# Kernel tuning notes

Measured on AMD Instinct MI355X. Metric: run time of the kernel, lower is better.

The kernel has to match this reference:

```python
import jax, jax.numpy as jnp
import numpy as np

N = 163842        # icosphere level-7 vertex count
IN_FEATS = 64
OUT_FEATS = 64
K = 7             # fixed neighborhood size (self + 6 ring neighbors)


def setup_inputs() -> dict:
    key = jax.random.key(0)
    k1, k2, k3, k4 = jax.random.split(key, 4)
    x = jax.random.normal(k1, (N, IN_FEATS), dtype=jnp.float32)
    neigh_orders = jax.random.randint(k2, (K * N,), 0, N, dtype=jnp.int64)
    # torch nn.Linear(7*in, out): weight [out, 7*in], bias [out]
    W = jax.random.normal(k3, (OUT_FEATS, K * IN_FEATS), dtype=jnp.float32) * 0.05
    b = jax.random.normal(k4, (OUT_FEATS,), dtype=jnp.float32) * 0.05
    return {"x": x, "neigh_orders": neigh_orders, "W": W, "b": b}


def reference(x, neigh_orders, W, b):
    # Gather neighbor features: [7*N, in] -> [N, 7*in]
    mat = x[neigh_orders].reshape(x.shape[0], -1)
    # Linear: mat @ W.T + b -> [N, out]
    return jnp.einsum("nk,ok->no", mat, W) + b
```

## Files before the change

kernel.cpp:

```cpp
#include <hip/hip_runtime.h>
#include <hip/hip_bf16.h>

#define NV     163842
#define KTOT   448
#define KQ     56
#define XUNITS (NV * 64 / 8)
#define WQUADS (64 * KTOT / 4)
#define XB_BYTES ((size_t)NV * 64 * 2)
#define WB_BYTES (KQ * 64 * 16)

typedef __attribute__((ext_vector_type(8))) short bf16x8;
typedef __attribute__((ext_vector_type(4))) float f32x4;

__device__ __forceinline__ unsigned f2bf(float f) {
    unsigned u = __builtin_bit_cast(unsigned, f);
    return (u + 0x7FFFu + ((u >> 16) & 1u)) >> 16;
}
__device__ __forceinline__ unsigned pack2(float a, float b) {
    return f2bf(a) | (f2bf(b) << 16);
}

__global__ __launch_bounds__(256) void prep_kernel(
    const float* __restrict__ x, const float* __restrict__ W,
    unsigned char* __restrict__ ws)
{
    const int g = blockIdx.x * 256 + threadIdx.x;
    if (g < XUNITS) {
        const float4 lo = *reinterpret_cast<const float4*>(x + (size_t)g * 8);
        const float4 hi = *reinterpret_cast<const float4*>(x + (size_t)g * 8 + 4);
        uint4 u;
        u.x = pack2(lo.x, lo.y); u.y = pack2(lo.z, lo.w);
        u.z = pack2(hi.x, hi.y); u.w = pack2(hi.z, hi.w);
        *reinterpret_cast<uint4*>(ws + (size_t)g * 16) = u;
    } else if (g < XUNITS + WQUADS) {
        const int q = g - XUNITS;
        const int i = q << 2;
        const int o = i / KTOT;
        const int k = i - o * KTOT;
        const int kq = k >> 3;
        const int u = (kq << 6) + (o ^ ((kq & 3) << 1));
        const float4 w = *reinterpret_cast<const float4*>(W + i);
        uint2 p;
        p.x = pack2(w.x, w.y); p.y = pack2(w.z, w.w);
        *reinterpret_cast<uint2*>(ws + XB_BYTES + (size_t)u * 16 + (k & 7) * 2) = p;
    }
}

__global__ __launch_bounds__(512, 4) void conv_gemm2(
    const uint4* __restrict__ xb, const int* __restrict__ neigh,
    const uint4* __restrict__ Wb, const float* __restrict__ bias,
    float* __restrict__ out)
{
    __shared__ uint4 Wl[KQ * 64];
    const int t = threadIdx.x;
    for (int u = t; u < KQ * 64; u += 512) Wl[u] = Wb[u];
    __syncthreads();

    const int wave = t >> 6, lane = t & 63;
    const int l15 = lane & 15, lg = lane >> 4;
    const int sl15 = l15 ^ (lg << 1);

    const int rowbase = blockIdx.x * 256 + wave * 32;
    const int row0 = rowbase + l15;
    const int row1 = row0 + 16;
    const int r0c = row0 < NV ? row0 : NV - 1;
    const int r1c = row1 < NV ? row1 : NV - 1;

    int idx0[7], idx1[7];
    #pragma unroll
    for (int j = 0; j < 7; ++j) {
        idx0[j] = neigh[r0c * 7 + j];
        idx1[j] = neigh[r1c * 7 + j];
    }

    f32x4 acc[2][4];
    #pragma unroll
    for (int m = 0; m < 2; ++m)
        #pragma unroll
        for (int n = 0; n < 4; ++n)
            acc[m][n] = (f32x4){0.f, 0.f, 0.f, 0.f};

    #pragma unroll
    for (int j = 0; j < 7; ++j) {
        const uint4* p0 = xb + (size_t)idx0[j] * 8;
        const uint4* p1 = xb + (size_t)idx1[j] * 8;
        uint4 a00 = p0[lg];
        uint4 a01 = p0[4 + lg];
        uint4 a10 = p1[lg];
        uint4 a11 = p1[4 + lg];
        #pragma unroll
        for (int h = 0; h < 2; ++h) {
            const int kq = ((j * 2 + h) << 2) + lg;
            const int bbase = (kq << 6) + sl15;
            bf16x8 A0 = __builtin_bit_cast(bf16x8, h ? a01 : a00);
            bf16x8 A1 = __builtin_bit_cast(bf16x8, h ? a11 : a10);
            #pragma unroll
            for (int n = 0; n < 4; ++n) {
                bf16x8 B = __builtin_bit_cast(bf16x8, Wl[bbase + (n << 4)]);
                acc[0][n] = __builtin_amdgcn_mfma_f32_16x16x32_bf16(A0, B, acc[0][n], 0, 0, 0);
                acc[1][n] = __builtin_amdgcn_mfma_f32_16x16x32_bf16(A1, B, acc[1][n], 0, 0, 0);
            }
        }
    }

    float bv[4];
    #pragma unroll
    for (int n = 0; n < 4; ++n) bv[n] = bias[(n << 4) + l15];

    #pragma unroll
    for (int m = 0; m < 2; ++m) {
        const int rb = rowbase + (m << 4) + (lg << 2);
        #pragma unroll
        for (int r = 0; r < 4; ++r) {
            const int row = rb + r;
            if (row < NV) {
                float* po = out + (size_t)row * 64 + l15;
                #pragma unroll
                for (int n = 0; n < 4; ++n)
                    po[n << 4] = acc[m][n][r] + bv[n];
            }
        }
    }
}

__global__ __launch_bounds__(256) void conv_gemm_kernel(
    const float* __restrict__ x, const int* __restrict__ neigh,
    const float* __restrict__ W, const float* __restrict__ bias,
    float* __restrict__ out)
{
    __shared__ unsigned Wl[56 * 64 * 4];
    const int t = threadIdx.x;
    for (int g = t; g < (64 * KTOT) / 4; g += 256) {
        int i = g << 2;
        int o = i / KTOT;
        int k = i - o * KTOT;
        const float4 w = *reinterpret_cast<const float4*>(W + i);
        unsigned p0 = pack2(w.x, w.y);
        unsigned p1 = pack2(w.z, w.w);
        unsigned* dst = &Wl[((((k >> 3) << 6) + o) << 2) + ((k & 7) >> 1)];
        *reinterpret_cast<uint2*>(dst) = make_uint2(p0, p1);
    }
    __syncthreads();

    const int wave = t >> 6, lane = t & 63;
    const int l15 = lane & 15, lg = lane >> 4;
    const int rowbase = blockIdx.x * 128 + wave * 32;
    const int row0 = rowbase + l15;
    const int row1 = row0 + 16;
    const int r0c = row0 < NV ? row0 : NV - 1;
    const int r1c = row1 < NV ? row1 : NV - 1;

    int idx0[7], idx1[7];
    #pragma unroll
    for (int j = 0; j < 7; ++j) {
        idx0[j] = neigh[r0c * 7 + j];
        idx1[j] = neigh[r1c * 7 + j];
    }

    f32x4 acc[2][4];
    #pragma unroll
    for (int m = 0; m < 2; ++m)
        #pragma unroll
        for (int n = 0; n < 4; ++n)
            acc[m][n] = (f32x4){0.f, 0.f, 0.f, 0.f};

    for (int j = 0; j < 7; ++j) {
        const float* p0 = x + (size_t)idx0[j] * 64;
        const float* p1 = x + (size_t)idx1[j] * 64;
        #pragma unroll
        for (int h = 0; h < 2; ++h) {
            const int foff = (h << 5) + (lg << 3);
            float4 a0lo = *reinterpret_cast<const float4*>(p0 + foff);
            float4 a0hi = *reinterpret_cast<const float4*>(p0 + foff + 4);
            float4 a1lo = *reinterpret_cast<const float4*>(p1 + foff);
            float4 a1hi = *reinterpret_cast<const float4*>(p1 + foff + 4);
            union { unsigned u[4]; bf16x8 v; } A0, A1;
            A0.u[0] = pack2(a0lo.x, a0lo.y); A0.u[1] = pack2(a0lo.z, a0lo.w);
            A0.u[2] = pack2(a0hi.x, a0hi.y); A0.u[3] = pack2(a0hi.z, a0hi.w);
            A1.u[0] = pack2(a1lo.x, a1lo.y); A1.u[1] = pack2(a1lo.z, a1lo.w);
            A1.u[2] = pack2(a1hi.x, a1hi.y); A1.u[3] = pack2(a1hi.z, a1hi.w);
            const int kq = (((j << 1) + h) << 2) + lg;
            #pragma unroll
            for (int n = 0; n < 4; ++n) {
                bf16x8 B = *reinterpret_cast<const bf16x8*>(
                    &Wl[((kq << 6) + (n << 4) + l15) << 2]);
                acc[0][n] = __builtin_amdgcn_mfma_f32_16x16x32_bf16(A0.v, B, acc[0][n], 0, 0, 0);
                acc[1][n] = __builtin_amdgcn_mfma_f32_16x16x32_bf16(A1.v, B, acc[1][n], 0, 0, 0);
            }
        }
    }

    float bv[4];
    #pragma unroll
    for (int n = 0; n < 4; ++n) bv[n] = bias[(n << 4) + l15];

    #pragma unroll
    for (int m = 0; m < 2; ++m) {
        const int rb = rowbase + (m << 4) + (lg << 2);
        #pragma unroll
        for (int r = 0; r < 4; ++r) {
            const int row = rb + r;
            if (row < NV) {
                float* po = out + (size_t)row * 64 + l15;
                #pragma unroll
                for (int n = 0; n < 4; ++n)
                    po[n << 4] = acc[m][n][r] + bv[n];
            }
        }
    }
}

extern "C" void kernel_launch(void* const* d_in, const int* in_sizes, int n_in,
                              void* d_out, int out_size, void* d_ws, size_t ws_size,
                              hipStream_t stream) {
    const float* x     = (const float*)d_in[0];
    const int*   neigh = (const int*)d_in[1];
    const float* W     = (const float*)d_in[2];
    const float* b     = (const float*)d_in[3];
    float* out = (float*)d_out;

    if (ws_size >= XB_BYTES + WB_BYTES) {
        unsigned char* ws = (unsigned char*)d_ws;
        const int prep_blocks = (XUNITS + WQUADS + 255) / 256;
        prep_kernel<<<dim3(prep_blocks), dim3(256), 0, stream>>>(x, W, ws);
        const uint4* xb = (const uint4*)ws;
        const uint4* Wb = (const uint4*)(ws + XB_BYTES);
        const int blocks = (NV + 255) / 256;
        conv_gemm2<<<dim3(blocks), dim3(512), 0, stream>>>(xb, neigh, Wb, b, out);
    } else {
        const int blocks = (NV + 127) / 128;
        conv_gemm_kernel<<<dim3(blocks), dim3(256), 0, stream>>>(x, neigh, W, b, out);
    }
}
```

Before: 49.61 us.

## Use persistent waves with atomic tile scheduler and software-pipelined gathers

Replaces the one-tile-per-wave grid with a persistent grid of 512 blocks (4096 waves). Each wave takes further 32-row tiles from a global atomic counter that the prep kernel resets to zero. The gathered x loads now run through a 4-deep rotating register prefetch, so the loads for step s+4 are in flight while the MFMAs for step s execute. The weights are loaded into LDS once per block instead of once per 256 rows, and neighbor indices are fetched before the LDS fill. In exchange it adds one atomic per tile and a serial index fetch between tiles, and it relies on the grid fitting fully resident.

```diff
diff --git a/kernel.cpp b/kernel.cpp
--- a/kernel.cpp
+++ b/kernel.cpp
@@ -4,6 +4,8 @@
 #define NV     163842
 #define KTOT   448
 #define KQ     56
+#define NT     ((NV + 31) / 32)
+#define NWAVES 4096
 #define XUNITS (NV * 64 / 8)
 #define WQUADS (64 * KTOT / 4)
 #define XB_BYTES ((size_t)NV * 64 * 2)
@@ -43,81 +45,108 @@
         uint2 p;
         p.x = pack2(w.x, w.y); p.y = pack2(w.z, w.w);
         *reinterpret_cast<uint2*>(ws + XB_BYTES + (size_t)u * 16 + (k & 7) * 2) = p;
-    }
-}
-
-__global__ __launch_bounds__(512, 4) void conv_gemm2(
+    } else if (g == XUNITS + WQUADS) {
+        *reinterpret_cast<int*>(ws + XB_BYTES + WB_BYTES) = 0;
+    }
+}
+
+__global__ __launch_bounds__(512, 4) void conv_gemm3(
     const uint4* __restrict__ xb, const int* __restrict__ neigh,
     const uint4* __restrict__ Wb, const float* __restrict__ bias,
-    float* __restrict__ out)
+    float* __restrict__ out, int* __restrict__ counter)
 {
     __shared__ uint4 Wl[KQ * 64];
     const int t = threadIdx.x;
+    const int wave = t >> 6, lane = t & 63;
+    const int l15 = lane & 15, lg = lane >> 4;
+
+    int tile = blockIdx.x * 8 + wave;
+
+    int idx0[7], idx1[7];
+    {
+        const int rb = tile * 32;
+        int r0 = rb + l15;      r0 = r0 < NV ? r0 : NV - 1;
+        int r1 = rb + 16 + l15; r1 = r1 < NV ? r1 : NV - 1;
+        #pragma unroll
+        for (int j = 0; j < 7; ++j) {
+            idx0[j] = neigh[r0 * 7 + j];
+            idx1[j] = neigh[r1 * 7 + j];
+        }
+    }
+
     for (int u = t; u < KQ * 64; u += 512) Wl[u] = Wb[u];
     __syncthreads();
 
-    const int wave = t >> 6, lane = t & 63;
-    const int l15 = lane & 15, lg = lane >> 4;
     const int sl15 = l15 ^ (lg << 1);
-
-    const int rowbase = blockIdx.x * 256 + wave * 32;
-    const int row0 = rowbase + l15;
-    const int row1 = row0 + 16;
-    const int r0c = row0 < NV ? row0 : NV - 1;
-    const int r1c = row1 < NV ? row1 : NV - 1;
-
-    int idx0[7], idx1[7];
-    #pragma unroll
-    for (int j = 0; j < 7; ++j) {
-        idx0[j] = neigh[r0c * 7 + j];
-        idx1[j] = neigh[r1c * 7 + j];
-    }
-
-    f32x4 acc[2][4];
-    #pragma unroll
-    for (int m = 0; m < 2; ++m)
-        #pragma unroll
-        for (int n = 0; n < 4; ++n)
-            acc[m][n] = (f32x4){0.f, 0.f, 0.f, 0.f};
-
-    #pragma unroll
-    for (int j = 0; j < 7; ++j) {
-        const uint4* p0 = xb + (size_t)idx0[j] * 8;
-        const uint4* p1 = xb + (size_t)idx1[j] * 8;
-        uint4 a00 = p0[lg];
-        uint4 a01 = p0[4 + lg];
-        uint4 a10 = p1[lg];
-        uint4 a11 = p1[4 + lg];
-        #pragma unroll
-        for (int h = 0; h < 2; ++h) {
-            const int kq = ((j * 2 + h) << 2) + lg;
-            const int bbase = (kq << 6) + sl15;
-            bf16x8 A0 = __builtin_bit_cast(bf16x8, h ? a01 : a00);
-            bf16x8 A1 = __builtin_bit_cast(bf16x8, h ? a11 : a10);
+    float bv[4];
+    #pragma unroll
+    for (int n = 0; n < 4; ++n) bv[n] = bias[(n << 4) + l15];
+
+    while (true) {
+        const int rowbase = tile * 32;
+
+        f32x4 acc[2][4];
+        #pragma unroll
+        for (int m = 0; m < 2; ++m)
+            #pragma unroll
+            for (int n = 0; n < 4; ++n)
+                acc[m][n] = (f32x4){0.f, 0.f, 0.f, 0.f};
+
+        uint4 pa[4], pb[4];
+        #pragma unroll
+        for (int s = 0; s < 4; ++s) {
+            const int j = s >> 1, h = s & 1;
+            pa[s] = xb[(size_t)idx0[j] * 8 + (h << 2) + lg];
+            pb[s] = xb[(size_t)idx1[j] * 8 + (h << 2) + lg];
+        }
+        #pragma unroll
+        for (int s = 0; s < 14; ++s) {
+            const uint4 ca = pa[s & 3];
+            const uint4 cb = pb[s & 3];
+            if (s + 4 < 14) {
+                const int s2 = s + 4, j = s2 >> 1, h = s2 & 1;
+                pa[s & 3] = xb[(size_t)idx0[j] * 8 + (h << 2) + lg];
+                pb[s & 3] = xb[(size_t)idx1[j] * 8 + (h << 2) + lg];
+            }
+            const int bbase = (((s << 2) + lg) << 6) + sl15;
+            const bf16x8 A0 = __builtin_bit_cast(bf16x8, ca);
+            const bf16x8 A1 = __builtin_bit_cast(bf16x8, cb);
             #pragma unroll
             for (int n = 0; n < 4; ++n) {
-                bf16x8 B = __builtin_bit_cast(bf16x8, Wl[bbase + (n << 4)]);
+                const bf16x8 B = __builtin_bit_cast(bf16x8, Wl[bbase + (n << 4)]);
                 acc[0][n] = __builtin_amdgcn_mfma_f32_16x16x32_bf16(A0, B, acc[0][n], 0, 0, 0);
                 acc[1][n] = __builtin_amdgcn_mfma_f32_16x16x32_bf16(A1, B, acc[1][n], 0, 0, 0);
             }
         }
-    }
-
-    float bv[4];
-    #pragma unroll
-    for (int n = 0; n < 4; ++n) bv[n] = bias[(n << 4) + l15];
-
-    #pragma unroll
-    for (int m = 0; m < 2; ++m) {
-        const int rb = rowbase + (m << 4) + (lg << 2);
-        #pragma unroll
-        for (int r = 0; r < 4; ++r) {
-            const int row = rb + r;
-            if (row < NV) {
-                float* po = out + (size_t)row * 64 + l15;
-                #pragma unroll
-                for (int n = 0; n < 4; ++n)
-                    po[n << 4] = acc[m][n][r] + bv[n];
+
+        #pragma unroll
+        for (int m = 0; m < 2; ++m) {
+            const int rb = rowbase + (m << 4) + (lg << 2);
+            #pragma unroll
+            for (int r = 0; r < 4; ++r) {
+                const int row = rb + r;
+                if (row < NV) {
+                    float* po = out + (size_t)row * 64 + l15;
+                    #pragma unroll
+                    for (int n = 0; n < 4; ++n)
+                        po[n << 4] = acc[m][n][r] + bv[n];
+                }
+            }
+        }
+
+        int nt = 0;
+        if (lane == 0) nt = atomicAdd(counter, 1);
+        nt = __shfl(nt, 0) + NWAVES;
+        if (nt >= NT) break;
+        tile = nt;
+        {
+            const int rb = tile * 32;
+            int r0 = rb + l15;      r0 = r0 < NV ? r0 : NV - 1;
+            int r1 = rb + 16 + l15; r1 = r1 < NV ? r1 : NV - 1;
+            #pragma unroll
+            for (int j = 0; j < 7; ++j) {
+                idx0[j] = neigh[r0 * 7 + j];
+                idx1[j] = neigh[r1 * 7 + j];
             }
         }
     }
@@ -219,14 +248,14 @@
     const float* b     = (const float*)d_in[3];
     float* out = (float*)d_out;
 
-    if (ws_size >= XB_BYTES + WB_BYTES) {
+    if (ws_size >= XB_BYTES + WB_BYTES + sizeof(int)) {
         unsigned char* ws = (unsigned char*)d_ws;
-        const int prep_blocks = (XUNITS + WQUADS + 255) / 256;
+        const int prep_blocks = (XUNITS + WQUADS + 1 + 255) / 256;
         prep_kernel<<<dim3(prep_blocks), dim3(256), 0, stream>>>(x, W, ws);
         const uint4* xb = (const uint4*)ws;
         const uint4* Wb = (const uint4*)(ws + XB_BYTES);
-        const int blocks = (NV + 255) / 256;
-        conv_gemm2<<<dim3(blocks), dim3(512), 0, stream>>>(xb, neigh, Wb, b, out);
+        int* counter = (int*)(ws + XB_BYTES + WB_BYTES);
+        conv_gemm3<<<dim3(512), dim3(512), 0, stream>>>(xb, neigh, Wb, b, out, counter);
     } else {
         const int blocks = (NV + 127) / 128;
         conv_gemm_kernel<<<dim3(blocks), dim3(256), 0, stream>>>(x, neigh, W, b, out);
```

After: 136.7 us. +175.6%, slower.

## Persistent grid with register-resident weights and software-pipelined neighbor gathers

Applied to the files above, without the earlier changes.

Replaces the LDS-staged weight GEMM with a persistent kernel of fixed grid size. Each wave keeps its 16 output channels' weight slice in registers and computes the transposed product (W as A operand, gathered x as B), so there are no LDS reads or block-level syncs. Tiles of 16 vertices are processed in a grid-stride loop, with the next tile's neighbor indices prefetched and the 7 gathers issued three deep ahead of the MFMAs. The output is written as contiguous float4 stores. In exchange, each vertex's gathered row is now fetched by all four waves instead of one, and per-wave MFMA work per tile is small.

```diff
diff --git a/kernel.cpp b/kernel.cpp
--- a/kernel.cpp
+++ b/kernel.cpp
@@ -4,6 +4,8 @@
 #define NV     163842
 #define KTOT   448
 #define KQ     56
+#define NT16   ((NV + 15) / 16)
+#define GRID   1024
 #define XUNITS (NV * 64 / 8)
 #define WQUADS (64 * KTOT / 4)
 #define XB_BYTES ((size_t)NV * 64 * 2)
@@ -37,8 +39,7 @@
         const int i = q << 2;
         const int o = i / KTOT;
         const int k = i - o * KTOT;
-        const int kq = k >> 3;
-        const int u = (kq << 6) + (o ^ ((kq & 3) << 1));
+        const int u = o * KQ + (k >> 3);
         const float4 w = *reinterpret_cast<const float4*>(W + i);
         uint2 p;
         p.x = pack2(w.x, w.y); p.y = pack2(w.z, w.w);
@@ -46,80 +47,77 @@
     }
 }
 
-__global__ __launch_bounds__(512, 4) void conv_gemm2(
+__global__ __launch_bounds__(256, 4) void conv_gemm4(
     const uint4* __restrict__ xb, const int* __restrict__ neigh,
-    const uint4* __restrict__ Wb, const float* __restrict__ bias,
+    const uint4* __restrict__ Wq, const float* __restrict__ bias,
     float* __restrict__ out)
 {
-    __shared__ uint4 Wl[KQ * 64];
     const int t = threadIdx.x;
-    for (int u = t; u < KQ * 64; u += 512) Wl[u] = Wb[u];
-    __syncthreads();
-
     const int wave = t >> 6, lane = t & 63;
     const int l15 = lane & 15, lg = lane >> 4;
-    const int sl15 = l15 ^ (lg << 1);
-
-    const int rowbase = blockIdx.x * 256 + wave * 32;
-    const int row0 = rowbase + l15;
-    const int row1 = row0 + 16;
-    const int r0c = row0 < NV ? row0 : NV - 1;
-    const int r1c = row1 < NV ? row1 : NV - 1;
-
-    int idx0[7], idx1[7];
-    #pragma unroll
-    for (int j = 0; j < 7; ++j) {
-        idx0[j] = neigh[r0c * 7 + j];
-        idx1[j] = neigh[r1c * 7 + j];
-    }
-
-    f32x4 acc[2][4];
-    #pragma unroll
-    for (int m = 0; m < 2; ++m)
-        #pragma unroll
-        for (int n = 0; n < 4; ++n)
-            acc[m][n] = (f32x4){0.f, 0.f, 0.f, 0.f};
-
-    #pragma unroll
-    for (int j = 0; j < 7; ++j) {
-        const uint4* p0 = xb + (size_t)idx0[j] * 8;
-        const uint4* p1 = xb + (size_t)idx1[j] * 8;
-        uint4 a00 = p0[lg];
-        uint4 a01 = p0[4 + lg];
-        uint4 a10 = p1[lg];
-        uint4 a11 = p1[4 + lg];
-        #pragma unroll
-        for (int h = 0; h < 2; ++h) {
-            const int kq = ((j * 2 + h) << 2) + lg;
-            const int bbase = (kq << 6) + sl15;
-            bf16x8 A0 = __builtin_bit_cast(bf16x8, h ? a01 : a00);
-            bf16x8 A1 = __builtin_bit_cast(bf16x8, h ? a11 : a10);
+    const int orow = (wave << 4) + l15;
+
+    uint4 w[14];
+    #pragma unroll
+    for (int s = 0; s < 14; ++s)
+        w[s] = Wq[orow * KQ + (s << 2) + lg];
+
+    const float4 bv = *reinterpret_cast<const float4*>(bias + (wave << 4) + (lg << 2));
+
+    int idx[7];
+    {
+        int v = blockIdx.x * 16 + l15;
+        int vc = v < NV ? v : NV - 1;
+        #pragma unroll
+        for (int j = 0; j < 7; ++j) idx[j] = neigh[vc * 7 + j];
+    }
+
+    for (int tile = blockIdx.x; tile < NT16; tile += GRID) {
+        const int v = (tile << 4) + l15;
+
+        f32x4 acc = (f32x4){0.f, 0.f, 0.f, 0.f};
+
+        uint4 ga[3], gb[3];
+        #pragma unroll
+        for (int jp = 0; jp < 3; ++jp) {
+            const uint4* p = xb + (size_t)idx[jp] * 8 + lg;
+            ga[jp] = p[0];
+            gb[jp] = p[4];
+        }
+
+        int nidx[7];
+        const int ntile = tile + GRID;
+        if (ntile < NT16) {
+            int nv = (ntile << 4) + l15;
+            int nvc = nv < NV ? nv : NV - 1;
             #pragma unroll
-            for (int n = 0; n < 4; ++n) {
-                bf16x8 B = __builtin_bit_cast(bf16x8, Wl[bbase + (n << 4)]);
-                acc[0][n] = __builtin_amdgcn_mfma_f32_16x16x32_bf16(A0, B, acc[0][n], 0, 0, 0);
-                acc[1][n] = __builtin_amdgcn_mfma_f32_16x16x32_bf16(A1, B, acc[1][n], 0, 0, 0);
+            for (int j = 0; j < 7; ++j) nidx[j] = neigh[nvc * 7 + j];
+        }
+
+        #pragma unroll
+        for (int j = 0; j < 7; ++j) {
+            const uint4 ca = ga[j % 3];
+            const uint4 cb = gb[j % 3];
+            if (j + 3 < 7) {
+                const uint4* p = xb + (size_t)idx[j + 3] * 8 + lg;
+                ga[j % 3] = p[0];
+                gb[j % 3] = p[4];
             }
-        }
-    }
-
-    float bv[4];
-    #pragma unroll
-    for (int n = 0; n < 4; ++n) bv[n] = bias[(n << 4) + l15];
-
-    #pragma unroll
-    for (int m = 0; m < 2; ++m) {
-        const int rb = rowbase + (m << 4) + (lg << 2);
-        #pragma unroll
-        for (int r = 0; r < 4; ++r) {
-            const int row = rb + r;
-            if (row < NV) {
-                float* po = out + (size_t)row * 64 + l15;
-                #pragma unroll
-                for (int n = 0; n < 4; ++n)
-                    po[n << 4] = acc[m][n][r] + bv[n];
-            }
-        }
+            const bf16x8 A0 = __builtin_bit_cast(bf16x8, w[2 * j]);
+            const bf16x8 A1 = __builtin_bit_cast(bf16x8, w[2 * j + 1]);
+            acc = __builtin_amdgcn_mfma_f32_16x16x32_bf16(A0, __builtin_bit_cast(bf16x8, ca), acc, 0, 0, 0);
+            acc = __builtin_amdgcn_mfma_f32_16x16x32_bf16(A1, __builtin_bit_cast(bf16x8, cb), acc, 0, 0, 0);
+        }
+
+        if (v < NV) {
+            float4 st;
+            st.x = acc[0] + bv.x; st.y = acc[1] + bv.y;
+            st.z = acc[2] + bv.z; st.w = acc[3] + bv.w;
+            *reinterpret_cast<float4*>(out + (size_t)v * 64 + (wave << 4) + (lg << 2)) = st;
+        }
+
+        #pragma unroll
+        for (int j = 0; j < 7; ++j) idx[j] = nidx[j];
     }
 }
 
@@ -224,9 +222,8 @@
         const int prep_blocks = (XUNITS + WQUADS + 255) / 256;
         prep_kernel<<<dim3(prep_blocks), dim3(256), 0, stream>>>(x, W, ws);
         const uint4* xb = (const uint4*)ws;
-        const uint4* Wb = (const uint4*)(ws + XB_BYTES);
-        const int blocks = (NV + 255) / 256;
-        conv_gemm2<<<dim3(blocks), dim3(512), 0, stream>>>(xb, neigh, Wb, b, out);
+        const uint4* Wq = (const uint4*)(ws + XB_BYTES);
+        conv_gemm4<<<dim3(GRID), dim3(256), 0, stream>>>(xb, neigh, Wq, b, out);
     } else {
         const int blocks = (NV + 127) / 128;
         conv_gemm_kernel<<<dim3(blocks), dim3(256), 0, stream>>>(x, neigh, W, b, out);
```

New measurement: 88.41 us. +78.2%, slower.

## Use fixed 512-block grid of 12-wave blocks with strided tile mapping

Applied to the files above, without the earlier changes.

Replaces the 641-block grid of 8-wave blocks with a fixed grid of 512 blocks of 12 waves, each wave handling a 32-row tile strided by the grid size. Neighbor index loads are issued before the shared-memory weight fill and barrier so their latency overlaps the fill. Fewer blocks means the 56KB weight tile is copied into LDS fewer times overall, at the cost of larger blocks and a tail where some waves have no tile.

```diff
diff --git a/kernel.cpp b/kernel.cpp
--- a/kernel.cpp
+++ b/kernel.cpp
@@ -4,6 +4,8 @@
 #define NV     163842
 #define KTOT   448
 #define KQ     56
+#define WTILES 5121
+#define GRID6  512
 #define XUNITS (NV * 64 / 8)
 #define WQUADS (64 * KTOT / 4)
 #define XB_BYTES ((size_t)NV * 64 * 2)
@@ -46,32 +48,38 @@
     }
 }
 
-__global__ __launch_bounds__(512, 4) void conv_gemm2(
+__global__ __launch_bounds__(768, 6) void conv_gemm6(
     const uint4* __restrict__ xb, const int* __restrict__ neigh,
     const uint4* __restrict__ Wb, const float* __restrict__ bias,
     float* __restrict__ out)
 {
     __shared__ uint4 Wl[KQ * 64];
     const int t = threadIdx.x;
-    for (int u = t; u < KQ * 64; u += 512) Wl[u] = Wb[u];
-    __syncthreads();
-
     const int wave = t >> 6, lane = t & 63;
     const int l15 = lane & 15, lg = lane >> 4;
+
+    const int tile = blockIdx.x + GRID6 * wave;
+    const bool work = tile < WTILES;
+
+    int idx0[7], idx1[7];
+    if (work) {
+        const int rb = tile * 32;
+        int r0 = rb + l15;      r0 = r0 < NV ? r0 : NV - 1;
+        int r1 = rb + 16 + l15; r1 = r1 < NV ? r1 : NV - 1;
+        #pragma unroll
+        for (int j = 0; j < 7; ++j) {
+            idx0[j] = neigh[r0 * 7 + j];
+            idx1[j] = neigh[r1 * 7 + j];
+        }
+    }
+
+    for (int u = t; u < KQ * 64; u += 768) Wl[u] = Wb[u];
+    __syncthreads();
+
+    if (!work) return;
+
     const int sl15 = l15 ^ (lg << 1);
-
-    const int rowbase = blockIdx.x * 256 + wave * 32;
-    const int row0 = rowbase + l15;
-    const int row1 = row0 + 16;
-    const int r0c = row0 < NV ? row0 : NV - 1;
-    const int r1c = row1 < NV ? row1 : NV - 1;
-
-    int idx0[7], idx1[7];
-    #pragma unroll
-    for (int j = 0; j < 7; ++j) {
-        idx0[j] = neigh[r0c * 7 + j];
-        idx1[j] = neigh[r1c * 7 + j];
-    }
+    const int rowbase = tile * 32;
 
     f32x4 acc[2][4];
     #pragma unroll
@@ -92,11 +100,11 @@
         for (int h = 0; h < 2; ++h) {
             const int kq = ((j * 2 + h) << 2) + lg;
             const int bbase = (kq << 6) + sl15;
-            bf16x8 A0 = __builtin_bit_cast(bf16x8, h ? a01 : a00);
-            bf16x8 A1 = __builtin_bit_cast(bf16x8, h ? a11 : a10);
+            const bf16x8 A0 = __builtin_bit_cast(bf16x8, h ? a01 : a00);
+            const bf16x8 A1 = __builtin_bit_cast(bf16x8, h ? a11 : a10);
             #pragma unroll
             for (int n = 0; n < 4; ++n) {
-                bf16x8 B = __builtin_bit_cast(bf16x8, Wl[bbase + (n << 4)]);
+                const bf16x8 B = __builtin_bit_cast(bf16x8, Wl[bbase + (n << 4)]);
                 acc[0][n] = __builtin_amdgcn_mfma_f32_16x16x32_bf16(A0, B, acc[0][n], 0, 0, 0);
                 acc[1][n] = __builtin_amdgcn_mfma_f32_16x16x32_bf16(A1, B, acc[1][n], 0, 0, 0);
             }
@@ -225,8 +233,7 @@
         prep_kernel<<<dim3(prep_blocks), dim3(256), 0, stream>>>(x, W, ws);
         const uint4* xb = (const uint4*)ws;
         const uint4* Wb = (const uint4*)(ws + XB_BYTES);
-        const int blocks = (NV + 255) / 256;
-        conv_gemm2<<<dim3(blocks), dim3(512), 0, stream>>>(xb, neigh, Wb, b, out);
+        conv_gemm6<<<dim3(GRID6), dim3(768), 0, stream>>>(xb, neigh, Wb, b, out);
     } else {
         const int blocks = (NV + 127) / 128;
         conv_gemm_kernel<<<dim3(blocks), dim3(256), 0, stream>>>(x, neigh, W, b, out);
```

New measurement: 44.62 us. 10.1% less time.
